# Kernel tuning notes

Measured on AMD Instinct MI355X. Metric: run time of the kernel, lower is better.

Reference implementation:

```python
import jax, jax.numpy as jnp
import numpy as np

TEMPERATURE = 0.2
EPS = 1e-8  # torch F.cosine_similarity eps


def setup_inputs() -> dict:
    key = jax.random.key(0)
    k1, k2, k3 = jax.random.split(key, 3)
    N, D, K = 2048, 512, 65536
    query = jax.random.normal(k1, (N, D), dtype=jnp.float32)
    keys = jax.random.normal(k2, (N, D), dtype=jnp.float32)
    queue = jax.random.normal(k3, (K, D), dtype=jnp.float32)
    return {"query": query, "keys": keys, "queue": queue}


def reference(query, keys, queue):
    # Norms
    qn = jnp.linalg.norm(query, axis=-1)   # [N]
    kn = jnp.linalg.norm(keys, axis=-1)    # [N]
    un = jnp.linalg.norm(queue, axis=-1)   # [K]
    # Positive logits: only the diagonal of the NxN cosine-sim is used,
    # so compute row-wise dot products directly.  [N]
    l_pos = jnp.sum(query * keys, axis=-1) / jnp.maximum(qn * kn, EPS) / TEMPERATURE
    # Negative logits via GEMM then normalize.  [N, K]
    l_neg = jnp.einsum('nd,kd->nk', query, queue)
    l_neg = l_neg / jnp.maximum(qn[:, None] * un[None, :], EPS) / TEMPERATURE
    # logits = [l_pos | l_neg], labels are all 0 -> CE = mean(logsumexp - logit_0)
    logits = jnp.concatenate([l_pos[:, None], l_neg], axis=1)  # [N, K+1]
    lse = jax.nn.logsumexp(logits, axis=1)                     # [N]
    loss = jnp.mean(lse - l_pos)
    return loss
```

## Files before the change

kernel.cpp:

```cpp
#include <hip/hip_runtime.h>
#include <hip/hip_bf16.h>
#include <math.h>

#define N_ROWS 2048
#define D_DIM  512
#define K_NEG  65536
#define INV_T  5.0f
#define NC     4
#define NT     (NC * 16)

typedef __bf16 bf16x8 __attribute__((ext_vector_type(8)));
typedef float  f32x4  __attribute__((ext_vector_type(4)));

__device__ __forceinline__ void gload_lds16(const __bf16* g, __bf16* l) {
    __builtin_amdgcn_global_load_lds(
        (const __attribute__((address_space(1))) void*)g,
        (__attribute__((address_space(3))) void*)l, 16, 0, 0);
}

__global__ __launch_bounds__(256) void prep_all_kernel(
    const float* __restrict__ query, const float* __restrict__ keys,
    const float* __restrict__ queue,
    __bf16* __restrict__ Abf, __bf16* __restrict__ Bbf,
    float* __restrict__ sq, float* __restrict__ ru,
    float* __restrict__ lpos, float* __restrict__ rowsum) {
    const int lane = threadIdx.x & 63;
    if (blockIdx.x < N_ROWS / 4) {
        const int row = blockIdx.x * 4 + (threadIdx.x >> 6);
        const float4* qv = reinterpret_cast<const float4*>(query + (size_t)row * D_DIM) + lane * 2;
        const float4* kv = reinterpret_cast<const float4*>(keys  + (size_t)row * D_DIM) + lane * 2;
        float4 q0 = qv[0], q1 = qv[1];
        float4 k0 = kv[0], k1 = kv[1];
        float ssq = q0.x*q0.x + q0.y*q0.y + q0.z*q0.z + q0.w*q0.w
                  + q1.x*q1.x + q1.y*q1.y + q1.z*q1.z + q1.w*q1.w;
        float ssk = k0.x*k0.x + k0.y*k0.y + k0.z*k0.z + k0.w*k0.w
                  + k1.x*k1.x + k1.y*k1.y + k1.z*k1.z + k1.w*k1.w;
        float dot = q0.x*k0.x + q0.y*k0.y + q0.z*k0.z + q0.w*k0.w
                  + q1.x*k1.x + q1.y*k1.y + q1.z*k1.z + q1.w*k1.w;
#pragma unroll
        for (int off = 32; off > 0; off >>= 1) {
            ssq += __shfl_xor(ssq, off, 64);
            ssk += __shfl_xor(ssk, off, 64);
            dot += __shfl_xor(dot, off, 64);
        }
        bf16x8 o;
        o[0] = (__bf16)q0.x; o[1] = (__bf16)q0.y; o[2] = (__bf16)q0.z; o[3] = (__bf16)q0.w;
        o[4] = (__bf16)q1.x; o[5] = (__bf16)q1.y; o[6] = (__bf16)q1.z; o[7] = (__bf16)q1.w;
        reinterpret_cast<bf16x8*>(Abf + (size_t)row * D_DIM)[lane] = o;
        if (lane == 0) {
            float qn = sqrtf(ssq), kn = sqrtf(ssk);
            float lp = dot / fmaxf(qn * kn, 1e-8f) * INV_T;
            sq[row]     = INV_T / fmaxf(qn, 1e-8f);
            lpos[row]   = lp;
            rowsum[row] = __expf(lp);
        }
    } else {
        const int row = (blockIdx.x - N_ROWS / 4) * 4 + (threadIdx.x >> 6);
        const float4* uv = reinterpret_cast<const float4*>(queue + (size_t)row * D_DIM) + lane * 2;
        float4 u0 = uv[0], u1 = uv[1];
        float ss = u0.x*u0.x + u0.y*u0.y + u0.z*u0.z + u0.w*u0.w
                 + u1.x*u1.x + u1.y*u1.y + u1.z*u1.z + u1.w*u1.w;
#pragma unroll
        for (int off = 32; off > 0; off >>= 1) ss += __shfl_xor(ss, off, 64);
        bf16x8 o;
        o[0] = (__bf16)u0.x; o[1] = (__bf16)u0.y; o[2] = (__bf16)u0.z; o[3] = (__bf16)u0.w;
        o[4] = (__bf16)u1.x; o[5] = (__bf16)u1.y; o[6] = (__bf16)u1.z; o[7] = (__bf16)u1.w;
        reinterpret_cast<bf16x8*>(Bbf + (size_t)row * D_DIM)[lane] = o;
        if (lane == 0) ru[row] = 1.0f / fmaxf(sqrtf(ss), 1e-8f);
    }
}

__global__ __launch_bounds__(256, 3) void gemm_exp_kernel(
    const __bf16* __restrict__ A, const __bf16* __restrict__ B,
    const float* __restrict__ sq, const float* __restrict__ ru,
    float* __restrict__ rowsum) {
    __shared__ __bf16 sA[2 * 4096];
    __shared__ __bf16 sB[2 * 4096];
    const int tid  = threadIdx.x;
    const int wave = tid >> 6, lane = tid & 63;
    const int rowBlock = blockIdx.x;
    const int colGroup = blockIdx.y;

    const int wm = wave >> 1, wn = wave & 1;
    const int q4 = lane >> 4, m16 = lane & 15;

    const int r4 = lane >> 2, c2 = lane & 3;
    const int gsw = c2 ^ ((r4 >> 1) & 3);
    const int j0 = wave, j1 = wave + 4;
    const __bf16* gA  = A + (((size_t)(rowBlock * 128 + r4)) << 9) + (gsw << 3);
    const __bf16* gB0 = B + (((size_t)(colGroup * NC * 128 + r4)) << 9) + (gsw << 3);
    const int rsw = (q4 ^ ((m16 >> 1) & 3)) << 3;

    float sqv[4][4];
#pragma unroll
    for (int i = 0; i < 4; ++i)
#pragma unroll
        for (int r = 0; r < 4; ++r)
            sqv[i][r] = sq[rowBlock * 128 + wm * 64 + i * 16 + q4 * 4 + r];

    float srow[4][4] = {{0.f,0.f,0.f,0.f},{0.f,0.f,0.f,0.f},
                        {0.f,0.f,0.f,0.f},{0.f,0.f,0.f,0.f}};
    f32x4 acc[4][4] = {};

#define STAGE(T, BUF) do {                                                        \
        const int cb_ = (T) >> 4, kof_ = ((T) & 15) * 32;                         \
        const __bf16* gBc_ = gB0 + ((size_t)cb_ << 16);                           \
        __bf16* dA_ = &sA[(BUF) * 4096];                                          \
        __bf16* dB_ = &sB[(BUF) * 4096];                                          \
        gload_lds16(gA  + (size_t)j0 * 16 * D_DIM + kof_, &dA_[j0 * 512]);        \
        gload_lds16(gA  + (size_t)j1 * 16 * D_DIM + kof_, &dA_[j1 * 512]);        \
        gload_lds16(gBc_ + (size_t)j0 * 16 * D_DIM + kof_, &dB_[j0 * 512]);       \
        gload_lds16(gBc_ + (size_t)j1 * 16 * D_DIM + kof_, &dB_[j1 * 512]);       \
    } while (0)

    STAGE(0, 0);

    for (int t = 0; t < NT; ++t) {
        const int cur = t & 1;
        __syncthreads();
        if (t + 1 < NT) STAGE(t + 1, cur ^ 1);

        const __bf16* bA = &sA[cur * 4096];
        const __bf16* bB = &sB[cur * 4096];
        bf16x8 af[4], bq[4];
#pragma unroll
        for (int i = 0; i < 4; ++i)
            af[i] = *reinterpret_cast<const bf16x8*>(&bA[(wm * 64 + i * 16 + m16) * 32 + rsw]);
#pragma unroll
        for (int j = 0; j < 4; ++j)
            bq[j] = *reinterpret_cast<const bf16x8*>(&bB[(wn * 64 + j * 16 + m16) * 32 + rsw]);
#pragma unroll
        for (int i = 0; i < 4; ++i)
#pragma unroll
            for (int j = 0; j < 4; ++j)
                acc[i][j] = __builtin_amdgcn_mfma_f32_16x16x32_bf16(af[i], bq[j], acc[i][j], 0, 0, 0);

        if ((t & 15) == 15) {
            const int colBlock = colGroup * NC + (t >> 4);
            float ruv[4];
#pragma unroll
            for (int j = 0; j < 4; ++j)
                ruv[j] = ru[colBlock * 128 + wn * 64 + j * 16 + m16];
#pragma unroll
            for (int i = 0; i < 4; ++i)
#pragma unroll
                for (int r = 0; r < 4; ++r) {
                    float s = 0.f;
#pragma unroll
                    for (int j = 0; j < 4; ++j)
                        s += __expf(acc[i][j][r] * sqv[i][r] * ruv[j]);
                    srow[i][r] += s;
                    acc[i][0][r] = 0.f; acc[i][1][r] = 0.f;
                    acc[i][2][r] = 0.f; acc[i][3][r] = 0.f;
                }
        }
    }
#undef STAGE

#pragma unroll
    for (int i = 0; i < 4; ++i)
#pragma unroll
        for (int r = 0; r < 4; ++r) {
            float s = srow[i][r];
#pragma unroll
            for (int off = 1; off < 16; off <<= 1)
                s += __shfl_xor(s, off, 64);
            if (m16 == 0) {
                const int grow = rowBlock * 128 + wm * 64 + i * 16 + q4 * 4 + r;
                atomicAdd(&rowsum[grow], s);
            }
        }
}

__global__ __launch_bounds__(256) void finalize_kernel(
    const float* __restrict__ rowsum, const float* __restrict__ lpos,
    float* __restrict__ out) {
    const int tid = threadIdx.x;
    float acc = 0.f;
    for (int n = tid; n < N_ROWS; n += 256)
        acc += __logf(rowsum[n]) - lpos[n];
#pragma unroll
    for (int off = 32; off > 0; off >>= 1) acc += __shfl_xor(acc, off, 64);
    __shared__ float red[4];
    if ((tid & 63) == 0) red[tid >> 6] = acc;
    __syncthreads();
    if (tid == 0) out[0] = (red[0] + red[1] + red[2] + red[3]) * (1.0f / (float)N_ROWS);
}

extern "C" void kernel_launch(void* const* d_in, const int* in_sizes, int n_in,
                              void* d_out, int out_size, void* d_ws, size_t ws_size,
                              hipStream_t stream) {
    const float* query = (const float*)d_in[0];
    const float* keys  = (const float*)d_in[1];
    const float* queue = (const float*)d_in[2];

    char* ws = (char*)d_ws;
    __bf16* Abf = (__bf16*)ws;  ws += (size_t)N_ROWS * D_DIM * sizeof(__bf16);
    __bf16* Bbf = (__bf16*)ws;  ws += (size_t)K_NEG  * D_DIM * sizeof(__bf16);
    float*  sq   = (float*)ws;  ws += (size_t)N_ROWS * sizeof(float);
    float*  ru   = (float*)ws;  ws += (size_t)K_NEG  * sizeof(float);
    float*  lpos = (float*)ws;  ws += (size_t)N_ROWS * sizeof(float);
    float*  rsum = (float*)ws;  ws += (size_t)N_ROWS * sizeof(float);

    prep_all_kernel<<<N_ROWS / 4 + K_NEG / 4, 256, 0, stream>>>(
        query, keys, queue, Abf, Bbf, sq, ru, lpos, rsum);
    gemm_exp_kernel<<<dim3(N_ROWS / 128, K_NEG / 128 / NC), 256, 0, stream>>>(
        Abf, Bbf, sq, ru, rsum);
    finalize_kernel<<<1, 256, 0, stream>>>(rsum, lpos, (float*)d_out);
}
```

Measured before the change: 382.1 us.

## Rewrite GEMM as 256x256 tile, 8-wave, K=64 staged ping-pong pipeline

Replaces the 128x128 tile (four column blocks per workgroup, K-step 32) with a 256x256 output tile per 512-thread workgroup and a K-step of 64. Loads and MFMAs are split into half-tile phases with explicit barriers, lgkmcnt/vmcnt waits and s_setprio, so global-to-LDS loads interleave with compute. The aim is higher arithmetic intensity and better overlap of memory with MFMA. In exchange it uses more LDS and registers and more barriers, and issues one atomic per row-chunk per column block.

```diff
diff --git a/kernel.cpp b/kernel.cpp
--- a/kernel.cpp
+++ b/kernel.cpp
@@ -6,8 +6,6 @@
 #define D_DIM  512
 #define K_NEG  65536
 #define INV_T  5.0f
-#define NC     4
-#define NT     (NC * 16)
 
 typedef __bf16 bf16x8 __attribute__((ext_vector_type(8)));
 typedef float  f32x4  __attribute__((ext_vector_type(4)));
@@ -70,106 +68,127 @@
     }
 }
 
-__global__ __launch_bounds__(256, 3) void gemm_exp_kernel(
+__global__ __launch_bounds__(512, 2) void gemm_exp_kernel(
     const __bf16* __restrict__ A, const __bf16* __restrict__ B,
     const float* __restrict__ sq, const float* __restrict__ ru,
     float* __restrict__ rowsum) {
-    __shared__ __bf16 sA[2 * 4096];
-    __shared__ __bf16 sB[2 * 4096];
+    __shared__ __bf16 sA[2 * 256 * 64];
+    __shared__ __bf16 sB[2 * 256 * 64];
     const int tid  = threadIdx.x;
     const int wave = tid >> 6, lane = tid & 63;
+    const int wm = wave >> 2, wn = wave & 3;
+    const int q4 = lane >> 4, m16 = lane & 15, m8 = m16 & 7;
     const int rowBlock = blockIdx.x;
-    const int colGroup = blockIdx.y;
-
-    const int wm = wave >> 1, wn = wave & 1;
-    const int q4 = lane >> 4, m16 = lane & 15;
-
-    const int r4 = lane >> 2, c2 = lane & 3;
-    const int gsw = c2 ^ ((r4 >> 1) & 3);
-    const int j0 = wave, j1 = wave + 4;
-    const __bf16* gA  = A + (((size_t)(rowBlock * 128 + r4)) << 9) + (gsw << 3);
-    const __bf16* gB0 = B + (((size_t)(colGroup * NC * 128 + r4)) << 9) + (gsw << 3);
-    const int rsw = (q4 ^ ((m16 >> 1) & 3)) << 3;
-
-    float sqv[4][4];
-#pragma unroll
-    for (int i = 0; i < 4; ++i)
-#pragma unroll
-        for (int r = 0; r < 4; ++r)
-            sqv[i][r] = sq[rowBlock * 128 + wm * 64 + i * 16 + q4 * 4 + r];
-
-    float srow[4][4] = {{0.f,0.f,0.f,0.f},{0.f,0.f,0.f,0.f},
-                        {0.f,0.f,0.f,0.f},{0.f,0.f,0.f,0.f}};
-    f32x4 acc[4][4] = {};
-
-#define STAGE(T, BUF) do {                                                        \
-        const int cb_ = (T) >> 4, kof_ = ((T) & 15) * 32;                         \
-        const __bf16* gBc_ = gB0 + ((size_t)cb_ << 16);                           \
-        __bf16* dA_ = &sA[(BUF) * 4096];                                          \
-        __bf16* dB_ = &sB[(BUF) * 4096];                                          \
-        gload_lds16(gA  + (size_t)j0 * 16 * D_DIM + kof_, &dA_[j0 * 512]);        \
-        gload_lds16(gA  + (size_t)j1 * 16 * D_DIM + kof_, &dA_[j1 * 512]);        \
-        gload_lds16(gBc_ + (size_t)j0 * 16 * D_DIM + kof_, &dB_[j0 * 512]);       \
-        gload_lds16(gBc_ + (size_t)j1 * 16 * D_DIM + kof_, &dB_[j1 * 512]);       \
-    } while (0)
-
-    STAGE(0, 0);
-
-    for (int t = 0; t < NT; ++t) {
-        const int cur = t & 1;
-        __syncthreads();
-        if (t + 1 < NT) STAGE(t + 1, cur ^ 1);
-
-        const __bf16* bA = &sA[cur * 4096];
-        const __bf16* bB = &sB[cur * 4096];
-        bf16x8 af[4], bq[4];
-#pragma unroll
-        for (int i = 0; i < 4; ++i)
-            af[i] = *reinterpret_cast<const bf16x8*>(&bA[(wm * 64 + i * 16 + m16) * 32 + rsw]);
-#pragma unroll
-        for (int j = 0; j < 4; ++j)
-            bq[j] = *reinterpret_cast<const bf16x8*>(&bB[(wn * 64 + j * 16 + m16) * 32 + rsw]);
-#pragma unroll
-        for (int i = 0; i < 4; ++i)
+    const int colBlock = blockIdx.y;
+
+    const int sr   = (wave << 3) + (lane >> 3);
+    const int csrc = (((lane & 7) ^ (lane >> 3)) << 3);
+    const __bf16* gA = A + (((size_t)(rowBlock * 256 + sr)) << 9) + csrc;
+    const __bf16* gB = B + (((size_t)(colBlock * 256 + sr)) << 9) + csrc;
+    __bf16* lA = sA + (wave << 9);
+    __bf16* lB = sB + (wave << 9);
+
+#define STG(g_, l_, s_, h_, q_, t_)                                           \
+    gload_lds16((g_) + ((((h_) * 128 + (q_) * 64) << 9) + ((t_) << 6)),       \
+                (l_) + (((s_) << 14) + (((h_) * 128 + (q_) * 64) << 6)))
+#define STG_HA(s_, h_, t_) do { STG(gA, lA, s_, h_, 0, t_); STG(gA, lA, s_, h_, 1, t_); } while (0)
+#define STG_HB(s_, h_, t_) do { STG(gB, lB, s_, h_, 0, t_); STG(gB, lB, s_, h_, 1, t_); } while (0)
+
+    const int aBase = (wm * 128 + m16) << 6;
+    const int bBase = (wn * 64 + m16) << 6;
+    const int chk0 = ((q4 ^ m8) << 3);
+    const int chk1 = (((4 + q4) ^ m8) << 3);
+
+    f32x4 acc[8][4] = {};
+    bf16x8 aF[8], bLo[4], bHi[4];
+
+#define LDS_A(s_, iH_)                                                                    \
+    { _Pragma("unroll") for (int i2 = 0; i2 < 4; ++i2) {                                  \
+        aF[i2 * 2 + 0] = *reinterpret_cast<const bf16x8*>(                                \
+            &sA[((s_) << 14) + aBase + ((iH_) * 4 + i2) * 1024 + chk0]);                  \
+        aF[i2 * 2 + 1] = *reinterpret_cast<const bf16x8*>(                                \
+            &sA[((s_) << 14) + aBase + ((iH_) * 4 + i2) * 1024 + chk1]); } }
+#define LDS_B(s_, jH_, dst_)                                                              \
+    { _Pragma("unroll") for (int j2 = 0; j2 < 2; ++j2) {                                  \
+        dst_[j2 * 2 + 0] = *reinterpret_cast<const bf16x8*>(                              \
+            &sB[((s_) << 14) + bBase + ((jH_) * 2 + j2) * 1024 + chk0]);                  \
+        dst_[j2 * 2 + 1] = *reinterpret_cast<const bf16x8*>(                              \
+            &sB[((s_) << 14) + bBase + ((jH_) * 2 + j2) * 1024 + chk1]); } }
+
+#define MMA(iH_, jH_, bX_)                                                                \
+    { __builtin_amdgcn_s_setprio(1);                                                      \
+      _Pragma("unroll") for (int i2 = 0; i2 < 4; ++i2)                                    \
+      _Pragma("unroll") for (int j2 = 0; j2 < 2; ++j2)                                    \
+      _Pragma("unroll") for (int kk = 0; kk < 2; ++kk)                                    \
+          acc[(iH_) * 4 + i2][(jH_) * 2 + j2] = __builtin_amdgcn_mfma_f32_16x16x32_bf16(  \
+              aF[i2 * 2 + kk], bX_[j2 * 2 + kk], acc[(iH_) * 4 + i2][(jH_) * 2 + j2],     \
+              0, 0, 0);                                                                   \
+      __builtin_amdgcn_s_setprio(0); }
+
+#define BAR   __builtin_amdgcn_s_barrier()
+#define LGKM0 do { asm volatile("s_waitcnt lgkmcnt(0)" ::: "memory");                     \
+                   __builtin_amdgcn_sched_barrier(0); } while (0)
+#define VM(n_) asm volatile("s_waitcnt vmcnt(" #n_ ")" ::: "memory")
+
+    STG_HA(0, 0, 0); STG_HA(0, 1, 0); STG_HB(0, 0, 0); STG_HB(0, 1, 0);
+    STG_HB(1, 0, 1); STG_HB(1, 1, 1);
+    VM(4); BAR;
+
+#define ITERATION(t1_, tn0_, tn1_, FULL_, PH4W_, PH8W_)                                   \
+    {  LDS_A(0, 0); LDS_B(0, 0, bLo); STG_HA(1, 0, t1_);                         \
+      BAR; LGKM0; MMA(0, 0, bLo); BAR;                                                    \
+       LDS_B(0, 1, bHi); STG_HA(1, 1, t1_);                                      \
+      BAR; LGKM0; MMA(0, 1, bHi); BAR;                                                    \
+       LDS_A(0, 1); if (FULL_) STG_HB(0, 0, tn0_);                               \
+      BAR; LGKM0; MMA(1, 0, bLo); BAR;                                                    \
+       if (FULL_) STG_HB(0, 1, tn0_);                                            \
+      BAR; LGKM0; MMA(1, 1, bHi); PH4W_; BAR;                                             \
+       LDS_A(1, 0); LDS_B(1, 0, bLo); if (FULL_) STG_HA(0, 0, tn0_);             \
+      BAR; LGKM0; MMA(0, 0, bLo); BAR;                                                    \
+       LDS_B(1, 1, bHi); if (FULL_) STG_HA(0, 1, tn0_);                          \
+      BAR; LGKM0; MMA(0, 1, bHi); BAR;                                                    \
+       LDS_A(1, 1); if (FULL_) STG_HB(1, 0, tn1_);                               \
+      BAR; LGKM0; MMA(1, 0, bLo); BAR;                                                    \
+       if (FULL_) STG_HB(1, 1, tn1_);                                            \
+      BAR; LGKM0; MMA(1, 1, bHi); PH8W_; BAR; }
+
+    ITERATION(1, 2, 3, 1, VM(4), VM(4));
+    ITERATION(3, 4, 5, 1, VM(4), VM(4));
+    ITERATION(5, 6, 7, 1, VM(4), VM(4));
+    ITERATION(7, 8, 9, 0, VM(0), ((void)0));
+
+#undef ITERATION
+#undef STG
+#undef STG_HA
+#undef STG_HB
+#undef LDS_A
+#undef LDS_B
+#undef MMA
+#undef BAR
+#undef LGKM0
+#undef VM
+
+    float ruv[4];
+#pragma unroll
+    for (int j = 0; j < 4; ++j)
+        ruv[j] = ru[colBlock * 256 + wn * 64 + j * 16 + m16];
+    const int growBase = rowBlock * 256 + wm * 128 + q4 * 4;
+#pragma unroll
+    for (int i = 0; i < 8; ++i) {
+#pragma unroll
+        for (int r = 0; r < 4; ++r) {
+            const int grow = growBase + i * 16 + r;
+            const float sv = sq[grow];
+            float s = 0.f;
 #pragma unroll
             for (int j = 0; j < 4; ++j)
-                acc[i][j] = __builtin_amdgcn_mfma_f32_16x16x32_bf16(af[i], bq[j], acc[i][j], 0, 0, 0);
-
-        if ((t & 15) == 15) {
-            const int colBlock = colGroup * NC + (t >> 4);
-            float ruv[4];
-#pragma unroll
-            for (int j = 0; j < 4; ++j)
-                ruv[j] = ru[colBlock * 128 + wn * 64 + j * 16 + m16];
-#pragma unroll
-            for (int i = 0; i < 4; ++i)
-#pragma unroll
-                for (int r = 0; r < 4; ++r) {
-                    float s = 0.f;
-#pragma unroll
-                    for (int j = 0; j < 4; ++j)
-                        s += __expf(acc[i][j][r] * sqv[i][r] * ruv[j]);
-                    srow[i][r] += s;
-                    acc[i][0][r] = 0.f; acc[i][1][r] = 0.f;
-                    acc[i][2][r] = 0.f; acc[i][3][r] = 0.f;
-                }
+                s += __expf(acc[i][j][r] * sv * ruv[j]);
+#pragma unroll
+            for (int off = 1; off < 16; off <<= 1)
+                s += __shfl_xor(s, off, 64);
+            if (m16 == 0) atomicAdd(&rowsum[grow], s);
         }
     }
-#undef STAGE
-
-#pragma unroll
-    for (int i = 0; i < 4; ++i)
-#pragma unroll
-        for (int r = 0; r < 4; ++r) {
-            float s = srow[i][r];
-#pragma unroll
-            for (int off = 1; off < 16; off <<= 1)
-                s += __shfl_xor(s, off, 64);
-            if (m16 == 0) {
-                const int grow = rowBlock * 128 + wm * 64 + i * 16 + q4 * 4 + r;
-                atomicAdd(&rowsum[grow], s);
-            }
-        }
 }
 
 __global__ __launch_bounds__(256) void finalize_kernel(
@@ -204,7 +223,7 @@
 
     prep_all_kernel<<<N_ROWS / 4 + K_NEG / 4, 256, 0, stream>>>(
         query, keys, queue, Abf, Bbf, sq, ru, lpos, rsum);
-    gemm_exp_kernel<<<dim3(N_ROWS / 128, K_NEG / 128 / NC), 256, 0, stream>>>(
+    gemm_exp_kernel<<<dim3(N_ROWS / 256, K_NEG / 256), 512, 0, stream>>>(
         Abf, Bbf, sq, ru, rsum);
     finalize_kernel<<<1, 256, 0, stream>>>(rsum, lpos, (float*)d_out);
 }
```

New measurement: 491.2 us. +28.5%, slower.
